# Kernel tuning notes

Hardware: AMD Instinct MI355X
Metric: run time of the kernel (lower is better)

## Reference

```python
import jax, jax.numpy as jnp
import numpy as np

B, S, D, HD, M, NH, DFF = 32, 512, 512, 512, 1000, 8, 2048
BETA = 0.5
DH = D // NH


def _make_seq(kt, km):
    # sorted event times, integer markers stored as floats (as in torch code);
    # last quarter of each sequence is padding with sentinel t = -1, marker = -1
    t = jnp.sort(jax.random.uniform(kt, (B, S)) * 100.0, axis=1)
    mk = jax.random.randint(km, (B, S), 0, M).astype(jnp.float32)
    valid = jnp.arange(S) < (3 * S // 4)
    t = jnp.where(valid, t, -1.0)
    mk = jnp.where(valid, mk, -1.0)
    return jnp.stack([t, mk], axis=-1)  # [B, S, 2]


def setup_inputs() -> dict:
    key = jax.random.key(0)
    ks = jax.random.split(key, 20)
    s = 0.02
    n = lambda k, shp: jax.random.normal(k, shp, dtype=jnp.float32) * s
    return {
        'x_H': _make_seq(ks[0], ks[1]),
        'x_F': _make_seq(ks[2], ks[3]),
        'W_m': n(ks[4], (D, M)),
        'W_t': n(ks[5], (D,)),
        'b_t': n(ks[6], (D,)),
        'Wq': n(ks[7], (D, D)),
        'Wk': n(ks[8], (D, D)),
        'Wv': n(ks[9], (D, D)),
        'Wo': n(ks[10], (D, D)),
        'W1': n(ks[11], (D, DFF)),
        'b1': jnp.zeros((DFF,), jnp.float32),
        'W2': n(ks[12], (DFF, D)),
        'b2': jnp.zeros((D,), jnp.float32),
        'Wp': n(ks[13], (D, HD)),
        'bp': jnp.zeros((HD,), jnp.float32),
        'W_out': n(ks[14], (2 * HD, M)),
        'b_out': jnp.zeros((M,), jnp.float32),
    }


def _embed(x, W_m, W_t, b_t):
    # out = beta * W_m[:, marker] + (1-beta) * (W_t * t + b_t); zeros when t < 0
    t = x[..., 0]                                         # [B, S]
    mk = jnp.clip(x[..., 1], 0, M - 1).astype(jnp.int32)  # [B, S]
    e = BETA * W_m.T[mk] + (1.0 - BETA) * (W_t * t[..., None] + b_t)
    return jnp.where((t >= 0)[..., None], e, 0.0), (t >= 0)


def _encoder(e, mask, Wq, Wk, Wv, Wo, W1, b1, W2, b2, Wp, bp):
    # masked multi-head self-attention encoder + masked mean pool -> [B, HD]
    q = (e @ Wq).reshape(B, S, NH, DH)
    k = (e @ Wk).reshape(B, S, NH, DH)
    v = (e @ Wv).reshape(B, S, NH, DH)
    scores = jnp.einsum('bqhd,bkhd->bhqk', q, k) / (DH ** 0.5)
    scores = jnp.where(mask[:, None, None, :], scores, -1e9)
    a = jax.nn.softmax(scores, axis=-1)
    o = jnp.einsum('bhqk,bkhd->bqhd', a, v).reshape(B, S, D) @ Wo
    h = e + o
    h = h + jax.nn.relu(h @ W1 + b1) @ W2 + b2
    mf = mask.astype(e.dtype)[..., None]
    pooled = (h * mf).sum(axis=1) / jnp.maximum(mf.sum(axis=1), 1.0)
    return pooled @ Wp + bp


def reference(x_H, x_F, W_m, W_t, b_t, Wq, Wk, Wv, Wo, W1, b1, W2, b2, Wp, bp, W_out, b_out):
    eH, mH = _embed(x_H, W_m, W_t, b_t)
    eF, mF = _embed(x_F, W_m, W_t, b_t)
    hH = _encoder(eH, mH, Wq, Wk, Wv, Wo, W1, b1, W2, b2, Wp, bp)
    hF = _encoder(eF, mF, Wq, Wk, Wv, Wo, W1, b1, W2, b2, Wp, bp)
    lam = jax.nn.softmax(jnp.concatenate([hH, hF], axis=1) @ W_out + b_out, axis=1)
    mu = jnp.argmax(lam, axis=1)
    return lam, mu
```

## Files before the change

kernel.cpp:

```cpp
#include <hip/hip_runtime.h>
#include <math.h>

#define BATCH 32
#define BB    64
#define SEQ  512
#define DIM  512
#define MM   1000
#define NHEAD 8
#define DHEAD 64
#define DFFN 2048
#define BROWS (BB * SEQ)

typedef __attribute__((ext_vector_type(8))) short short8;
typedef __attribute__((ext_vector_type(4))) float f32x4;

__device__ __forceinline__ ushort f2bf(float x) {
    unsigned u = __builtin_bit_cast(unsigned, x);
    unsigned r = (u + 0x7FFFu + ((u >> 16) & 1u)) >> 16;
    return (ushort)r;
}
__device__ __forceinline__ float bf2f(ushort h) {
    unsigned u = ((unsigned)h) << 16;
    return __builtin_bit_cast(float, u);
}
__device__ __forceinline__ unsigned cvtpk_bf16(float lo, float hi) {
    unsigned r;
    asm volatile("v_cvt_pk_bf16_f32 %0, %1, %2" : "=v"(r) : "v"(lo), "v"(hi));
    return r;
}

#define GL2LDS(g, s) __builtin_amdgcn_global_load_lds( \
    (const __attribute__((address_space(1))) unsigned int*)(g), \
    (__attribute__((address_space(3))) unsigned int*)(s), 16, 0, 0)

constexpr size_t OFF_WMT  = 0;
constexpr size_t OFF_MASK = 524288;
constexpr size_t OFF_POOL = 557056;
constexpr size_t OFF_HENC = 589824;
constexpr size_t OFF_LOG  = 622592;
constexpr size_t OFF_WQTH = 655360;
constexpr size_t OFF_W1TH = 1179648;
constexpr size_t OFF_W2TH = 1703936;
constexpr size_t OFF_EHI  = 2228224;
constexpr size_t OFF_QB   = 19005440;
constexpr size_t OFF_KB   = 27394048;
constexpr size_t OFF_VB   = 35782656;

__global__ __launch_bounds__(256)
void setup_all(const float* __restrict__ Wm,
               const float* __restrict__ Wq, const float* __restrict__ Wk,
               const float* __restrict__ Wv, const float* __restrict__ Wo,
               const float* __restrict__ W1, const float* __restrict__ W2,
               float* __restrict__ WmT, ushort* __restrict__ WqkvTh,
               ushort* __restrict__ W1Th, ushort* __restrict__ W2Th)
{
    __shared__ float tile[32][33];
    const int bid = blockIdx.x;
    const int tx = threadIdx.x & 31;
    const int ty = threadIdx.x >> 5;
    if (bid < 512) {
        int mx = (bid & 31) * 32, dy = (bid >> 5) * 32;
        for (int i = ty; i < 32; i += 8) {
            int d = dy + i, m = mx + tx;
            tile[i][tx] = (m < MM) ? Wm[(size_t)d * MM + m] : 0.f;
        }
        __syncthreads();
        for (int i = ty; i < 32; i += 8) {
            int m = mx + i, d = dy + tx;
            if (m < MM) WmT[(size_t)m * DIM + d] = tile[tx][i];
        }
    } else if (bid < 1536) {
        int id = bid - 512;
        int n0 = (id & 63) * 32, k0 = (id >> 6) * 32;
        const float* W = (n0 < 512) ? Wq : (n0 < 1024) ? Wk
                       : (n0 < 1536) ? Wv : Wo;
        int nc = n0 & 511;
        for (int i = ty; i < 32; i += 8)
            tile[i][tx] = W[(size_t)(k0 + i) * 512 + nc + tx];
        __syncthreads();
        for (int i = ty; i < 32; i += 8)
            WqkvTh[(size_t)(n0 + i) * 512 + k0 + tx] = f2bf(tile[tx][i]);
    } else if (bid < 2560) {
        int id = bid - 1536;
        int n0 = (id & 63) * 32, k0 = (id >> 6) * 32;
        for (int i = ty; i < 32; i += 8)
            tile[i][tx] = W1[(size_t)(k0 + i) * DFFN + n0 + tx];
        __syncthreads();
        for (int i = ty; i < 32; i += 8)
            W1Th[(size_t)(n0 + i) * DIM + k0 + tx] = f2bf(tile[tx][i]);
    } else {
        int id = bid - 2560;
        int n0 = (id & 15) * 32, k0 = (id >> 4) * 32;
        for (int i = ty; i < 32; i += 8)
            tile[i][tx] = W2[(size_t)(k0 + i) * DIM + n0 + tx];
        __syncthreads();
        for (int i = ty; i < 32; i += 8)
            W2Th[(size_t)(n0 + i) * DFFN + k0 + tx] = f2bf(tile[tx][i]);
    }
}

__global__ __launch_bounds__(256)
void embed_kernel(const float* __restrict__ xH, const float* __restrict__ xF,
                  const float* __restrict__ WmT, const float* __restrict__ Wt,
                  const float* __restrict__ bt,
                  ushort* __restrict__ ehi, float* __restrict__ maskA)
{
    int sub  = threadIdx.x >> 6;
    int lane = threadIdx.x & 63;
    int bs   = blockIdx.x * 4 + sub;
    const float* xp = (bs < BATCH * SEQ) ? (xH + (size_t)bs * 2)
                                         : (xF + (size_t)(bs - BATCH * SEQ) * 2);
    float t   = xp[0];
    float mkf = xp[1];
    int   mk  = (int)fminf(fmaxf(mkf, 0.f), (float)(MM - 1));
    bool  valid = (t >= 0.f);
    if (lane == 0) maskA[bs] = valid ? 1.f : 0.f;
    const float* wrow = WmT + (size_t)mk * DIM + lane * 8;
    float4 w0 = *reinterpret_cast<const float4*>(wrow);
    float4 w1 = *reinterpret_cast<const float4*>(wrow + 4);
    float4 t0 = *reinterpret_cast<const float4*>(Wt + lane * 8);
    float4 t1 = *reinterpret_cast<const float4*>(Wt + lane * 8 + 4);
    float4 b0 = *reinterpret_cast<const float4*>(bt + lane * 8);
    float4 b1 = *reinterpret_cast<const float4*>(bt + lane * 8 + 4);
    float v[8];
    v[0] = w0.x * 0.5f + 0.5f * (t0.x * t + b0.x);
    v[1] = w0.y * 0.5f + 0.5f * (t0.y * t + b0.y);
    v[2] = w0.z * 0.5f + 0.5f * (t0.z * t + b0.z);
    v[3] = w0.w * 0.5f + 0.5f * (t0.w * t + b0.w);
    v[4] = w1.x * 0.5f + 0.5f * (t1.x * t + b1.x);
    v[5] = w1.y * 0.5f + 0.5f * (t1.y * t + b1.y);
    v[6] = w1.z * 0.5f + 0.5f * (t1.z * t + b1.z);
    v[7] = w1.w * 0.5f + 0.5f * (t1.w * t + b1.w);
    union { uint4 u; ushort s[8]; } ph;
    #pragma unroll
    for (int j = 0; j < 8; ++j)
        ph.s[j] = f2bf(valid ? v[j] : 0.f);
    *reinterpret_cast<uint4*>(ehi + (size_t)bs * DIM + lane * 8) = ph.u;
}

template<bool BIAS, bool RELU, bool RES, bool TRIPLE>
__global__ __launch_bounds__(256)
void gemm_bf16(const ushort* __restrict__ A0, const ushort* __restrict__ B0,
               const float* __restrict__ bias, const ushort* __restrict__ Rh,
               ushort* __restrict__ Oh, ushort* __restrict__ Ol,
               ushort* __restrict__ Ot,
               int Md, int Nd, int Kd, int lda, int ldb,
               const float* __restrict__ mrow)
{
    __shared__ __align__(16) ushort As[2][128 * 64];
    __shared__ __align__(16) ushort Bs[2][128 * 64];
    const int tid = threadIdx.x;
    const int w = tid >> 6, l = tid & 63;
    const int wr = w >> 1, wc = w & 1;
    const int l15 = l & 15, lg = l >> 4;
    const int id  = blockIdx.x + gridDim.x * blockIdx.y;
    const int nwg = gridDim.x * gridDim.y;
    const int qc  = nwg >> 3;
    const int lin = (id & 7) * qc + (id >> 3);
    const int row0 = (lin / gridDim.x) * 128;
    const int col0 = (lin % gridDim.x) * 128;
    const int lrow   = l >> 3;
    const int gchunk = (l & 7) ^ lrow;

    if (mrow) {
        float mv = (tid < 128) ? mrow[row0 + tid] : 0.f;
        if (!__syncthreads_or(mv != 0.f)) return;
    }

    f32x4 acc[4][4];
    #pragma unroll
    for (int m = 0; m < 4; m++)
        #pragma unroll
        for (int n = 0; n < 4; n++)
            acc[m][n] = (f32x4){0.f, 0.f, 0.f, 0.f};

    const int NT = Kd >> 6;
    int skt = 0;

    auto stage = [&](int bi) {
        ushort* Asb = &As[bi][0];
        ushort* Bsb = &Bs[bi][0];
        #pragma unroll
        for (int r = 0; r < 4; ++r) {
            int rowb = w * 32 + r * 8;
            int row  = rowb + lrow;
            GL2LDS(A0 + (size_t)(row0 + row) * lda + skt + gchunk * 8,
                   Asb + rowb * 64);
            GL2LDS(B0 + (size_t)(col0 + row) * ldb + skt + gchunk * 8,
                   Bsb + rowb * 64);
        }
        skt += 64;
    };

    stage(0);
    __syncthreads();

    for (int t = 0; t < NT; ++t) {
        const int cur = t & 1;
        if (t + 1 < NT) stage(cur ^ 1);
        const char* AsB = (const char*)&As[cur][0];
        const char* BsB = (const char*)&Bs[cur][0];
        #pragma unroll
        for (int ks = 0; ks < 2; ++ks) {
            const int g = ks * 4 + lg;
            short8 af[4], bfr[4];
            #pragma unroll
            for (int m = 0; m < 4; ++m) {
                int row = wr * 64 + m * 16 + l15;
                af[m] = *reinterpret_cast<const short8*>(
                    AsB + row * 128 + ((g ^ (row & 7)) << 4));
            }
            #pragma unroll
            for (int n = 0; n < 4; ++n) {
                int row = wc * 64 + n * 16 + l15;
                bfr[n] = *reinterpret_cast<const short8*>(
                    BsB + row * 128 + ((g ^ (row & 7)) << 4));
            }
            #pragma unroll
            for (int m = 0; m < 4; ++m)
                #pragma unroll
                for (int n = 0; n < 4; ++n)
                    acc[m][n] = __builtin_amdgcn_mfma_f32_16x16x32_bf16(
                        af[m], bfr[n], acc[m][n], 0, 0, 0);
        }
        __syncthreads();
    }

    #pragma unroll
    for (int m = 0; m < 4; ++m) {
        #pragma unroll
        for (int n = 0; n < 4; ++n) {
            int col = col0 + wc * 64 + n * 16 + l15;
            if (TRIPLE) {
                if (col0 < 512) {
                    #pragma unroll
                    for (int j = 0; j < 4; ++j) {
                        int row = row0 + wr * 64 + m * 16 + lg * 4 + j;
                        Oh[(size_t)row * 512 + col] = f2bf(acc[m][n][j]);
                    }
                } else if (col0 < 1024) {
                    #pragma unroll
                    for (int j = 0; j < 4; ++j) {
                        int row = row0 + wr * 64 + m * 16 + lg * 4 + j;
                        Ol[(size_t)row * 512 + (col - 512)] = f2bf(acc[m][n][j]);
                    }
                } else {
                    union { uint2 u; ushort s4[4]; } pk;
                    #pragma unroll
                    for (int j = 0; j < 4; ++j) pk.s4[j] = f2bf(acc[m][n][j]);
                    int brow = row0 + wr * 64 + m * 16 + lg * 4;
                    size_t idx = ((size_t)(brow >> 9) << 18)
                               + (size_t)(col - 1024) * SEQ + (brow & 511);
                    *reinterpret_cast<uint2*>(Ot + idx) = pk.u;
                }
            } else {
                float bia = 0.f;
                if (BIAS) bia = bias[col];
                #pragma unroll
                for (int j = 0; j < 4; ++j) {
                    int row = row0 + wr * 64 + m * 16 + lg * 4 + j;
                    size_t idx = (size_t)row * Nd + col;
                    float v = acc[m][n][j] + bia;
                    if (RES)  v += bf2f(Rh[idx]);
                    if (RELU) v = fmaxf(v, 0.f);
                    Oh[idx] = f2bf(v);
                }
            }
        }
    }
}

__global__ __launch_bounds__(512)
void attn_mfma(ushort* __restrict__ QO, const ushort* __restrict__ K,
               const ushort* __restrict__ Vt, const float* __restrict__ maskA)
{
    __shared__ __align__(16) ushort Ks[2][64 * 64];
    __shared__ __align__(16) ushort Vs[2][64 * 64];
    __shared__ __align__(16) ushort Pl[8][16 * 64];
    __shared__ float ms[512];
    const int h   = blockIdx.x;
    const int b   = blockIdx.y;
    const int qt  = blockIdx.z;
    const int tid = threadIdx.x;
    const int w = tid >> 6, l = tid & 63;
    const int l15 = l & 15, lg = l >> 4, l7 = l & 7;
    const int lrow   = l >> 3;
    const int gchunk = (l & 7) ^ lrow;
    const int qbase = qt * 128;

    #pragma unroll
    for (int rr = 0; rr < 2; ++rr) {
        int rowb = rr * 64 + w * 8;
        GL2LDS(QO + ((size_t)(b * SEQ + qbase + rowb + lrow)) * DIM
                  + h * DHEAD + gchunk * 8,
               &Pl[0][0] + rowb * 64);
    }
    ms[tid] = maskA[b * SEQ + tid];
    float qm = (tid < 128) ? maskA[b * SEQ + qbase + tid] : 0.f;
    if (!__syncthreads_or(qm != 0.f)) return;

    unsigned hbits = 0;
    #pragma unroll
    for (int t = 0; t < 8; ++t) {
        int mine = (tid < 64) ? (ms[t * 64 + tid] != 0.f) : 0;
        if (__syncthreads_or(mine)) hbits |= (1u << t);
    }

    short8 af[2];
    #pragma unroll
    for (int s = 0; s < 2; ++s) {
        int q = w * 16 + l15;
        int c = (s * 4 + lg) ^ l7;
        af[s] = *reinterpret_cast<const short8*>(&Pl[0][0] + q * 64 + c * 8);
    }

    short8 bones;
    #pragma unroll
    for (int i = 0; i < 8; ++i) bones[i] = (short)0x3F80;

    f32x4 oacc[4];
    #pragma unroll
    for (int t = 0; t < 4; ++t) oacc[t] = (f32x4){0.f, 0.f, 0.f, 0.f};
    f32x4 lacc = (f32x4){0.f, 0.f, 0.f, 0.f};

    ushort* pw = &Pl[w][0];

    auto stagekv = [&](int t, int bi) {
        int kv0 = t * 64;
        GL2LDS(K + ((size_t)(b * SEQ + kv0 + w * 8 + lrow)) * DIM
                 + h * DHEAD + gchunk * 8,
               &Ks[bi][0] + w * 8 * 64);
        GL2LDS(Vt + ((size_t)b << 18) + (size_t)(h * DHEAD + w * 8 + lrow) * SEQ
                  + kv0 + gchunk * 8,
               &Vs[bi][0] + w * 8 * 64);
    };

    int t0 = 0;
    while (t0 < 8 && !(hbits & (1u << t0))) ++t0;
    stagekv(t0, 0);
    __syncthreads();
    int cur = 0;
    for (int t = t0; t < 8; ) {
        int tn = t + 1;
        while (tn < 8 && !(hbits & (1u << tn))) ++tn;
        if (tn < 8) stagekv(tn, cur ^ 1);

        f32x4 sacc[4];
        #pragma unroll
        for (int t4 = 0; t4 < 4; ++t4) sacc[t4] = (f32x4){0.f, 0.f, 0.f, 0.f};
        #pragma unroll
        for (int s = 0; s < 2; ++s) {
            int c = (s * 4 + lg) ^ l7;
            #pragma unroll
            for (int t4 = 0; t4 < 4; ++t4) {
                int kv = t4 * 16 + l15;
                short8 bf = *reinterpret_cast<const short8*>(
                    &Ks[cur][0] + kv * 64 + c * 8);
                sacc[t4] = __builtin_amdgcn_mfma_f32_16x16x32_bf16(af[s], bf, sacc[t4], 0, 0, 0);
            }
        }

        float mk[4];
        #pragma unroll
        for (int t4 = 0; t4 < 4; ++t4) mk[t4] = ms[t * 64 + t4 * 16 + l15];
        #pragma unroll
        for (int t4 = 0; t4 < 4; ++t4)
            #pragma unroll
            for (int j = 0; j < 4; ++j)
                sacc[t4][j] = mk[t4] * __expf(sacc[t4][j] * 0.125f);

        #pragma unroll
        for (int t4 = 0; t4 < 4; ++t4) {
            int kvh = t4 * 16 + l15;
            int base = (kvh & 7);
            int hi3  = (kvh >> 3);
            #pragma unroll
            for (int jp = 0; jp < 4; jp += 2) {
                unsigned u = cvtpk_bf16(sacc[t4][jp], sacc[t4][jp + 1]);
                int q0 = lg * 4 + jp;
                int q1 = q0 + 1;
                pw[q0 * 64 + base + ((hi3 ^ (q0 & 7)) << 3)] = (ushort)u;
                pw[q1 * 64 + base + ((hi3 ^ (q1 & 7)) << 3)] = (ushort)(u >> 16);
            }
        }

        #pragma unroll
        for (int s = 0; s < 2; ++s) {
            int c = (s * 4 + lg) ^ l7;
            short8 pa = *reinterpret_cast<const short8*>(&pw[l15 * 64 + c * 8]);
            lacc = __builtin_amdgcn_mfma_f32_16x16x32_bf16(pa, bones, lacc, 0, 0, 0);
            #pragma unroll
            for (int dt = 0; dt < 4; ++dt) {
                int dh = dt * 16 + l15;
                short8 vb = *reinterpret_cast<const short8*>(
                    &Vs[cur][0] + dh * 64 + c * 8);
                oacc[dt] = __builtin_amdgcn_mfma_f32_16x16x32_bf16(pa, vb, oacc[dt], 0, 0, 0);
            }
        }

        __syncthreads();
        cur ^= 1;
        t = tn;
    }

    float inv[4];
    #pragma unroll
    for (int j = 0; j < 4; ++j) inv[j] = 1.0f / lacc[j];
    #pragma unroll
    for (int t = 0; t < 4; ++t) {
        #pragma unroll
        for (int j = 0; j < 4; ++j) {
            size_t g = ((size_t)(b * SEQ + qbase + w * 16 + lg * 4 + j)) * DIM
                     + h * DHEAD + t * 16 + l15;
            QO[g] = f2bf(oacc[t][j] * inv[j]);
        }
    }
}

__global__ __launch_bounds__(512)
void pool_kernel(const ushort* __restrict__ hh,
                 const float* __restrict__ maskA, float* __restrict__ pooled)
{
    int b  = blockIdx.x;
    int dq = blockIdx.y;
    int dl = threadIdx.x & 31;
    int sg = threadIdx.x >> 5;
    int d  = dq * 64 + dl * 2;
    float a0 = 0.f, a1 = 0.f, cnt = 0.f;
    for (int s = sg; s < SEQ; s += 16) {
        float mv = maskA[b * SEQ + s];
        if (mv == 0.f) continue;
        unsigned vh = *reinterpret_cast<const unsigned*>(
            &hh[((size_t)(b * SEQ + s)) * DIM + d]);
        a0 += bf2f((ushort)(vh & 0xffff));
        a1 += bf2f((ushort)(vh >> 16));
        cnt += 1.f;
    }
    __shared__ float r0[16][32];
    __shared__ float r1[16][32];
    __shared__ float rc[16];
    r0[sg][dl] = a0;
    r1[sg][dl] = a1;
    if (dl == 0) rc[sg] = cnt;
    __syncthreads();
    if (sg == 0) {
        float t0 = 0.f, t1 = 0.f, c = 0.f;
        #pragma unroll
        for (int g = 0; g < 16; ++g) { t0 += r0[g][dl]; t1 += r1[g][dl]; c += rc[g]; }
        float invc = 1.0f / fmaxf(c, 1.f);
        pooled[b * DIM + d]     = t0 * invc;
        pooled[b * DIM + d + 1] = t1 * invc;
    }
}

__global__ __launch_bounds__(512)
void proj_kernel(const float* __restrict__ pooled, const float* __restrict__ Wp,
                 const float* __restrict__ bp, float* __restrict__ henc)
{
    int b = blockIdx.x;
    int j = threadIdx.x;
    __shared__ float p[DIM];
    p[j] = pooled[b * DIM + j];
    __syncthreads();
    float a0 = 0.f, a1 = 0.f, a2 = 0.f, a3 = 0.f;
    for (int d = 0; d < DIM; d += 4) {
        a0 += p[d]     * Wp[(size_t)d       * DIM + j];
        a1 += p[d + 1] * Wp[(size_t)(d + 1) * DIM + j];
        a2 += p[d + 2] * Wp[(size_t)(d + 2) * DIM + j];
        a3 += p[d + 3] * Wp[(size_t)(d + 3) * DIM + j];
    }
    henc[(size_t)b * DIM + j] = ((a0 + a1) + (a2 + a3)) + bp[j];
}

__global__ __launch_bounds__(256)
void logits_kernel(const float* __restrict__ henc, const float* __restrict__ Wout,
                   const float* __restrict__ bout, float* __restrict__ logits)
{
    int b = blockIdx.y;
    int m = blockIdx.x * 256 + threadIdx.x;
    __shared__ float hh[2 * DIM];
    for (int j = threadIdx.x; j < DIM; j += 256) {
        hh[j]       = henc[(size_t)b * DIM + j];
        hh[DIM + j] = henc[(size_t)(BATCH + b) * DIM + j];
    }
    __syncthreads();
    if (m < MM) {
        float a0 = 0.f, a1 = 0.f, a2 = 0.f, a3 = 0.f;
        for (int j = 0; j < 2 * DIM; j += 4) {
            a0 += hh[j]     * Wout[(size_t)j       * MM + m];
            a1 += hh[j + 1] * Wout[(size_t)(j + 1) * MM + m];
            a2 += hh[j + 2] * Wout[(size_t)(j + 2) * MM + m];
            a3 += hh[j + 3] * Wout[(size_t)(j + 3) * MM + m];
        }
        logits[b * MM + m] = ((a0 + a1) + (a2 + a3)) + bout[m];
    }
}

__global__ __launch_bounds__(256)
void smax_kernel(const float* __restrict__ logits, float* __restrict__ out)
{
    int b   = blockIdx.x;
    int tid = threadIdx.x;
    __shared__ float red[256];
    __shared__ int   redi[256];

    float v[4];
    float mx = -INFINITY;
    #pragma unroll
    for (int i = 0; i < 4; i++) {
        int m = tid + i * 256;
        if (m < MM) { v[i] = logits[b * MM + m]; mx = fmaxf(mx, v[i]); }
        else v[i] = -INFINITY;
    }
    red[tid] = mx; __syncthreads();
    for (int st = 128; st > 0; st >>= 1) {
        if (tid < st) red[tid] = fmaxf(red[tid], red[tid + st]);
        __syncthreads();
    }
    mx = red[0]; __syncthreads();

    float sum = 0.f;
    #pragma unroll
    for (int i = 0; i < 4; i++) {
        int m = tid + i * 256;
        if (m < MM) { v[i] = expf(v[i] - mx); sum += v[i]; }
    }
    red[tid] = sum; __syncthreads();
    for (int st = 128; st > 0; st >>= 1) {
        if (tid < st) red[tid] += red[tid + st];
        __syncthreads();
    }
    float inv = 1.0f / red[0]; __syncthreads();

    float bestv = -INFINITY; int besti = 0x7fffffff;
    #pragma unroll
    for (int i = 0; i < 4; i++) {
        int m = tid + i * 256;
        if (m < MM) {
            float lam = v[i] * inv;
            out[b * MM + m] = lam;
            if (lam > bestv) { bestv = lam; besti = m; }
        }
    }
    red[tid] = bestv; redi[tid] = besti; __syncthreads();
    for (int st = 128; st > 0; st >>= 1) {
        if (tid < st) {
            float ov = red[tid + st]; int oi = redi[tid + st];
            if (ov > red[tid] || (ov == red[tid] && oi < redi[tid])) {
                red[tid] = ov; redi[tid] = oi;
            }
        }
        __syncthreads();
    }
    if (tid == 0) out[BATCH * MM + b] = (float)redi[0];
}

extern "C" void kernel_launch(void* const* d_in, const int* in_sizes, int n_in,
                              void* d_out, int out_size, void* d_ws, size_t ws_size,
                              hipStream_t stream)
{
    const float* xH   = (const float*)d_in[0];
    const float* xF   = (const float*)d_in[1];
    const float* Wm   = (const float*)d_in[2];
    const float* Wt   = (const float*)d_in[3];
    const float* bt   = (const float*)d_in[4];
    const float* Wq   = (const float*)d_in[5];
    const float* Wk   = (const float*)d_in[6];
    const float* Wv   = (const float*)d_in[7];
    const float* Wo   = (const float*)d_in[8];
    const float* W1   = (const float*)d_in[9];
    const float* b1   = (const float*)d_in[10];
    const float* W2   = (const float*)d_in[11];
    const float* b2   = (const float*)d_in[12];
    const float* Wp   = (const float*)d_in[13];
    const float* bp   = (const float*)d_in[14];
    const float* Wout = (const float*)d_in[15];
    const float* bout = (const float*)d_in[16];
    float* out = (float*)d_out;

    float* ws     = (float*)d_ws;
    float*  WmT    = ws + OFF_WMT;
    float*  maskA  = ws + OFF_MASK;
    float*  pooled = ws + OFF_POOL;
    float*  henc   = ws + OFF_HENC;
    float*  logits = ws + OFF_LOG;
    ushort* WqkvTh = (ushort*)(ws + OFF_WQTH);
    ushort* WoTh   = WqkvTh + (size_t)1536 * 512;
    ushort* W1Th   = (ushort*)(ws + OFF_W1TH);
    ushort* W2Th   = (ushort*)(ws + OFF_W2TH);
    ushort* ehi    = (ushort*)(ws + OFF_EHI);
    ushort* Qb     = (ushort*)(ws + OFF_QB);
    ushort* Kb     = (ushort*)(ws + OFF_KB);
    ushort* Vtb    = (ushort*)(ws + OFF_VB);
    ushort* rbuf   = (ushort*)(ws + OFF_KB);

    setup_all<<<dim3(3584), 256, 0, stream>>>(
        Wm, Wq, Wk, Wv, Wo, W1, W2, WmT, WqkvTh, W1Th, W2Th);

    embed_kernel<<<dim3(BROWS / 4), 256, 0, stream>>>(
        xH, xF, WmT, Wt, bt, ehi, maskA);
    gemm_bf16<false,false,false,true><<<dim3(12, 256), 256, 0, stream>>>(
        ehi, WqkvTh, nullptr, nullptr,
        Qb, Kb, Vtb, BROWS, 512, DIM, DIM, DIM, maskA);
    attn_mfma<<<dim3(NHEAD, BB, 4), 512, 0, stream>>>(Qb, Kb, Vtb, maskA);
    gemm_bf16<false,false,true,false><<<dim3(4, 256), 256, 0, stream>>>(
        Qb, WoTh, nullptr, ehi,
        ehi, nullptr, nullptr, BROWS, DIM, DIM, DIM, DIM, maskA);
    gemm_bf16<true,true,false,false><<<dim3(16, 256), 256, 0, stream>>>(
        ehi, W1Th, b1, nullptr,
        rbuf, nullptr, nullptr, BROWS, DFFN, DIM, DIM, DIM, maskA);
    gemm_bf16<true,false,true,false><<<dim3(4, 256), 256, 0, stream>>>(
        rbuf, W2Th, b2, ehi,
        Qb, nullptr, nullptr, BROWS, DIM, DFFN, DFFN, DFFN, maskA);
    pool_kernel<<<dim3(BB, 8), 512, 0, stream>>>(Qb, maskA, pooled);
    proj_kernel<<<dim3(BB), 512, 0, stream>>>(pooled, Wp, bp, henc);
    logits_kernel<<<dim3(4, BATCH), 256, 0, stream>>>(henc, Wout, bout, logits);
    smax_kernel<<<dim3(BATCH), 256, 0, stream>>>(logits, out);
}
```

Baseline: 368.8 us.

## Fuse masked mean-pool into final FFN GEMM epilogue, drop pool kernel

The last GEMM (W2 plus bias plus residual) no longer writes the full bf16 hidden state. Each tile instead reduces its rows, weighted by the row mask, into per-column partial sums using LDS atomics. It writes one 128-column partial per batch quarter into a small buffer, and fully masked tiles write zeros. proj_kernel then adds the four partials, computes the valid-row count, and divides. This removes a large activation write, the separate pool kernel's read of it, and one launch. The cost is shared-memory atomics in the epilogue and a different summation order.

```diff
diff --git a/kernel.cpp b/kernel.cpp
--- a/kernel.cpp
+++ b/kernel.cpp
@@ -42,6 +42,7 @@
 constexpr size_t OFF_W1TH = 1179648;
 constexpr size_t OFF_W2TH = 1703936;
 constexpr size_t OFF_EHI  = 2228224;
+constexpr size_t OFF_PPART= 10616832;
 constexpr size_t OFF_QB   = 19005440;
 constexpr size_t OFF_KB   = 27394048;
 constexpr size_t OFF_VB   = 35782656;
@@ -138,17 +139,19 @@
     *reinterpret_cast<uint4*>(ehi + (size_t)bs * DIM + lane * 8) = ph.u;
 }
 
-template<bool BIAS, bool RELU, bool RES, bool TRIPLE>
+template<bool BIAS, bool RELU, bool RES, bool TRIPLE, bool POOLF>
 __global__ __launch_bounds__(256)
 void gemm_bf16(const ushort* __restrict__ A0, const ushort* __restrict__ B0,
                const float* __restrict__ bias, const ushort* __restrict__ Rh,
                ushort* __restrict__ Oh, ushort* __restrict__ Ol,
-               ushort* __restrict__ Ot,
+               ushort* __restrict__ Ot, float* __restrict__ pPart,
                int Md, int Nd, int Kd, int lda, int ldb,
                const float* __restrict__ mrow)
 {
     __shared__ __align__(16) ushort As[2][128 * 64];
     __shared__ __align__(16) ushort Bs[2][128 * 64];
+    __shared__ float msk[128];
+    __shared__ float poolred[128];
     const int tid = threadIdx.x;
     const int w = tid >> 6, l = tid & 63;
     const int wr = w >> 1, wc = w & 1;
@@ -164,7 +167,13 @@
 
     if (mrow) {
         float mv = (tid < 128) ? mrow[row0 + tid] : 0.f;
-        if (!__syncthreads_or(mv != 0.f)) return;
+        if (tid < 128 && POOLF) msk[tid] = mv;
+        if (!__syncthreads_or(mv != 0.f)) {
+            if (POOLF && tid < 128)
+                pPart[(((size_t)((row0 >> 7) & 3)) * 64 + (row0 >> 9)) * 512
+                      + col0 + tid] = 0.f;
+            return;
+        }
     }
 
     f32x4 acc[4][4];
@@ -224,6 +233,34 @@
                         af[m], bfr[n], acc[m][n], 0, 0, 0);
         }
         __syncthreads();
+    }
+
+    if (POOLF) {
+        if (tid < 128) poolred[tid] = 0.f;
+        __syncthreads();
+        #pragma unroll
+        for (int n = 0; n < 4; ++n) {
+            int colloc = wc * 64 + n * 16 + l15;
+            int col = col0 + colloc;
+            float bia = BIAS ? bias[col] : 0.f;
+            float p = 0.f;
+            #pragma unroll
+            for (int m = 0; m < 4; ++m) {
+                #pragma unroll
+                for (int j = 0; j < 4; ++j) {
+                    int rowloc = wr * 64 + m * 16 + lg * 4 + j;
+                    float v = acc[m][n][j] + bia;
+                    if (RES) v += bf2f(Rh[(size_t)(row0 + rowloc) * Nd + col]);
+                    p += v * msk[rowloc];
+                }
+            }
+            atomicAdd(&poolred[colloc], p);
+        }
+        __syncthreads();
+        if (tid < 128)
+            pPart[(((size_t)((row0 >> 7) & 3)) * 64 + (row0 >> 9)) * 512
+                  + col0 + tid] = poolred[tid];
+        return;
     }
 
     #pragma unroll
@@ -418,49 +455,27 @@
 }
 
 __global__ __launch_bounds__(512)
-void pool_kernel(const ushort* __restrict__ hh,
-                 const float* __restrict__ maskA, float* __restrict__ pooled)
-{
-    int b  = blockIdx.x;
-    int dq = blockIdx.y;
-    int dl = threadIdx.x & 31;
-    int sg = threadIdx.x >> 5;
-    int d  = dq * 64 + dl * 2;
-    float a0 = 0.f, a1 = 0.f, cnt = 0.f;
-    for (int s = sg; s < SEQ; s += 16) {
-        float mv = maskA[b * SEQ + s];
-        if (mv == 0.f) continue;
-        unsigned vh = *reinterpret_cast<const unsigned*>(
-            &hh[((size_t)(b * SEQ + s)) * DIM + d]);
-        a0 += bf2f((ushort)(vh & 0xffff));
-        a1 += bf2f((ushort)(vh >> 16));
-        cnt += 1.f;
-    }
-    __shared__ float r0[16][32];
-    __shared__ float r1[16][32];
-    __shared__ float rc[16];
-    r0[sg][dl] = a0;
-    r1[sg][dl] = a1;
-    if (dl == 0) rc[sg] = cnt;
-    __syncthreads();
-    if (sg == 0) {
-        float t0 = 0.f, t1 = 0.f, c = 0.f;
-        #pragma unroll
-        for (int g = 0; g < 16; ++g) { t0 += r0[g][dl]; t1 += r1[g][dl]; c += rc[g]; }
-        float invc = 1.0f / fmaxf(c, 1.f);
-        pooled[b * DIM + d]     = t0 * invc;
-        pooled[b * DIM + d + 1] = t1 * invc;
-    }
-}
-
-__global__ __launch_bounds__(512)
-void proj_kernel(const float* __restrict__ pooled, const float* __restrict__ Wp,
-                 const float* __restrict__ bp, float* __restrict__ henc)
+void proj_kernel(const float* __restrict__ pPart, const float* __restrict__ maskA,
+                 const float* __restrict__ Wp, const float* __restrict__ bp,
+                 float* __restrict__ henc)
 {
     int b = blockIdx.x;
     int j = threadIdx.x;
     __shared__ float p[DIM];
-    p[j] = pooled[b * DIM + j];
+    __shared__ float cs[512];
+    cs[j] = maskA[b * SEQ + j];
+    __syncthreads();
+    for (int st = 256; st > 0; st >>= 1) {
+        if (j < st) cs[j] += cs[j + st];
+        __syncthreads();
+    }
+    float invc = 1.0f / fmaxf(cs[0], 1.f);
+    __syncthreads();
+    float s = pPart[((size_t)0 * 64 + b) * 512 + j]
+            + pPart[((size_t)1 * 64 + b) * 512 + j]
+            + pPart[((size_t)2 * 64 + b) * 512 + j]
+            + pPart[((size_t)3 * 64 + b) * 512 + j];
+    p[j] = s * invc;
     __syncthreads();
     float a0 = 0.f, a1 = 0.f, a2 = 0.f, a3 = 0.f;
     for (int d = 0; d < DIM; d += 4) {
@@ -581,9 +596,9 @@
     float* ws     = (float*)d_ws;
     float*  WmT    = ws + OFF_WMT;
     float*  maskA  = ws + OFF_MASK;
-    float*  pooled = ws + OFF_POOL;
     float*  henc   = ws + OFF_HENC;
     float*  logits = ws + OFF_LOG;
+    float*  pPart  = ws + OFF_PPART;
     ushort* WqkvTh = (ushort*)(ws + OFF_WQTH);
     ushort* WoTh   = WqkvTh + (size_t)1536 * 512;
     ushort* W1Th   = (ushort*)(ws + OFF_W1TH);
@@ -599,21 +614,20 @@
 
     embed_kernel<<<dim3(BROWS / 4), 256, 0, stream>>>(
         xH, xF, WmT, Wt, bt, ehi, maskA);
-    gemm_bf16<false,false,false,true><<<dim3(12, 256), 256, 0, stream>>>(
+    gemm_bf16<false,false,false,true,false><<<dim3(12, 256), 256, 0, stream>>>(
         ehi, WqkvTh, nullptr, nullptr,
-        Qb, Kb, Vtb, BROWS, 512, DIM, DIM, DIM, maskA);
+        Qb, Kb, Vtb, nullptr, BROWS, 512, DIM, DIM, DIM, maskA);
     attn_mfma<<<dim3(NHEAD, BB, 4), 512, 0, stream>>>(Qb, Kb, Vtb, maskA);
-    gemm_bf16<false,false,true,false><<<dim3(4, 256), 256, 0, stream>>>(
+    gemm_bf16<false,false,true,false,false><<<dim3(4, 256), 256, 0, stream>>>(
         Qb, WoTh, nullptr, ehi,
-        ehi, nullptr, nullptr, BROWS, DIM, DIM, DIM, DIM, maskA);
-    gemm_bf16<true,true,false,false><<<dim3(16, 256), 256, 0, stream>>>(
+        ehi, nullptr, nullptr, nullptr, BROWS, DIM, DIM, DIM, DIM, maskA);
+    gemm_bf16<true,true,false,false,false><<<dim3(16, 256), 256, 0, stream>>>(
         ehi, W1Th, b1, nullptr,
-        rbuf, nullptr, nullptr, BROWS, DFFN, DIM, DIM, DIM, maskA);
-    gemm_bf16<true,false,true,false><<<dim3(4, 256), 256, 0, stream>>>(
+        rbuf, nullptr, nullptr, nullptr, BROWS, DFFN, DIM, DIM, DIM, maskA);
+    gemm_bf16<true,false,true,false,true><<<dim3(4, 256), 256, 0, stream>>>(
         rbuf, W2Th, b2, ehi,
-        Qb, nullptr, nullptr, BROWS, DIM, DFFN, DFFN, DFFN, maskA);
-    pool_kernel<<<dim3(BB, 8), 512, 0, stream>>>(Qb, maskA, pooled);
-    proj_kernel<<<dim3(BB), 512, 0, stream>>>(pooled, Wp, bp, henc);
+        nullptr, nullptr, nullptr, pPart, BROWS, DIM, DFFN, DFFN, DFFN, maskA);
+    proj_kernel<<<dim3(BB), 512, 0, stream>>>(pPart, maskA, Wp, bp, henc);
     logits_kernel<<<dim3(4, BATCH), 256, 0, stream>>>(henc, Wout, bout, logits);
     smax_kernel<<<dim3(BATCH), 256, 0, stream>>>(logits, out);
 }
```

After: 353.3 us. -4.2%, faster.
